# Kernel tuning notes

Measured on AMD Instinct MI355X. Metric: run time of the kernel, lower is better.

The kernel has to match this reference:

```python
import jax, jax.numpy as jnp
import numpy as np
import math

BLUR_RADIUS = 2.0


def _disk_kernel(radius):
    r = int(math.ceil(radius))
    ys, xs = np.mgrid[-r:r + 1, -r:r + 1]
    d = np.sqrt(xs * xs + ys * ys)
    w = np.clip(radius + 0.5 - d, 0.0, 1.0)
    w = w / w.sum()
    return jnp.asarray(w[None, None], jnp.float32)  # [1,1,k,k]


def transform_points(h, p, eps=1e-8):
    # h: [B,3,3], p: [P,2] -> [B,P,2]
    ph = jnp.concatenate([p, jnp.ones_like(p[:, :1])], axis=-1)
    pt = jnp.einsum('pj,bij->bpi', ph, h)
    z = pt[..., 2:]
    scale = jnp.where(jnp.abs(z) > eps, 1.0 / (z + eps), jnp.ones_like(z))
    return scale * pt[..., :2]


def grid_sample(img, grid):
    # img [C,Hi,Wi], grid [H,W,2] normalized, bilinear, zeros padding, align_corners=False
    C, Hi, Wi = img.shape
    gx = (grid[..., 0] + 1.0) * (Wi * 0.5) - 0.5
    gy = (grid[..., 1] + 1.0) * (Hi * 0.5) - 0.5
    x0 = jnp.floor(gx)
    y0 = jnp.floor(gy)
    wx = gx - x0
    wy = gy - y0

    def tap(xf, yf):
        ok = ((xf >= 0) & (xf < Wi) & (yf >= 0) & (yf < Hi)).astype(img.dtype)
        xi = jnp.clip(xf.astype(jnp.int32), 0, Wi - 1)
        yi = jnp.clip(yf.astype(jnp.int32), 0, Hi - 1)
        return img[:, yi, xi] * ok

    return (tap(x0, y0) * (1 - wx) * (1 - wy) + tap(x0 + 1, y0) * wx * (1 - wy)
            + tap(x0, y0 + 1) * (1 - wx) * wy + tap(x0 + 1, y0 + 1) * wx * wy)


def draw_patches(patches, homos, scale, kernel, H, W):
    n, c = patches.shape[:2]
    k = kernel.shape[-1]
    margin = k // 2
    corners = jnp.array([[-1., -1.], [1., -1.], [1., 1.], [-1., 1.]], jnp.float32)
    tpts = transform_points(homos, corners)  # [n,4,2]
    img_max = jnp.array([W, H], jnp.float32)
    lo = jnp.clip(jnp.min(tpts, axis=1) - margin, 0.0, img_max)  # [n,2] (x,y)
    hi = jnp.clip(jnp.max(tpts, axis=1) + margin, 0.0, img_max)
    # nearest upsample by static integer scale
    up = jnp.repeat(jnp.repeat(patches, scale, axis=2), scale, axis=3)
    alpha = jnp.ones_like(up)
    p = 2 * margin
    dw = jnp.broadcast_to(kernel, (c, 1, k, k))
    conv = lambda x: jax.lax.conv_general_dilated(x, dw, (1, 1), 'VALID', feature_group_count=c)
    fp = conv(jnp.pad(up, ((0, 0), (0, 0), (p, p), (p, p)), mode='edge'))
    fa = conv(jnp.pad(alpha, ((0, 0), (0, 0), (p, p), (p, p))))
    Hf, Wf = fp.shape[-2], fp.shape[-1]
    smtx = jnp.diag(jnp.array([(Wf - 2 * margin) / Wf, (Hf - 2 * margin) / Hf, 1.0], jnp.float32))
    hinv_s = jnp.einsum('ij,njk->nik', smtx, jnp.linalg.inv(homos))
    ys, xs = jnp.meshgrid(jnp.arange(H, dtype=jnp.float32), jnp.arange(W, dtype=jnp.float32), indexing='ij')
    coord = jnp.stack([xs + 0.5, ys + 0.5], axis=-1)  # [H,W,2]
    grid = transform_points(hinv_s, coord.reshape(-1, 2)).reshape(n, H, W, 2)
    ix0 = jnp.floor(lo).astype(jnp.int32)
    ix1 = jnp.floor(hi).astype(jnp.int32)
    xi = jnp.arange(W)
    yi = jnp.arange(H)
    inb = ((xi[None, None, :] >= ix0[:, None, None, 0]) & (xi[None, None, :] < ix1[:, None, None, 0])
           & (yi[None, :, None] >= ix0[:, None, None, 1]) & (yi[None, :, None] < ix1[:, None, None, 1]))
    grid = jnp.where(inb[..., None], grid, -2.0)  # -2 -> out of range -> zeros
    placed = jax.vmap(grid_sample)(fp, grid)
    palpha = jax.vmap(grid_sample)(fa, grid)
    return placed, palpha


def tdot(a, b):
    return jnp.sum(a * b, axis=1, keepdims=True)


def tnorm(m, eps=1e-8):
    l = jnp.maximum(jnp.sqrt(jnp.sum(m * m, axis=1, keepdims=True)), eps)
    return m / l


def render_specular(light_dir, view_dir, normals, roughness, fresnel=0.1, eps=1e-8):
    hv = tnorm((light_dir + view_dir) * 0.5, eps)
    NoH = jax.nn.relu(tdot(normals, hv))
    NoV = jax.nn.relu(tdot(normals, view_dir))
    NoL = jax.nn.relu(tdot(normals, light_dir))
    VoH = jax.nn.relu(tdot(view_dir, hv))
    alpha = roughness * roughness
    tmp = alpha / jnp.maximum(NoH * NoH * (alpha * alpha - 1.0) + 1.0, eps)
    D = tmp * tmp * (1.0 / np.pi)
    kk = alpha * 0.5
    G = NoL * NoV / jnp.maximum((NoL * (1.0 - kk) + kk) * (NoV * (1.0 - kk) + kk), eps)
    coeff = VoH * (-5.55473 * VoH - 6.98316)
    F_term = fresnel + (1.0 - fresnel) * jnp.exp2(coeff)
    f_s = D * G * F_term / jnp.maximum(4.0 * NoL * NoV, eps)
    return f_s * NoL * np.pi


def _unit(k, shape):
    v = jax.random.normal(k, shape, jnp.float32)
    return v / jnp.maximum(jnp.linalg.norm(v, axis=-1, keepdims=True), 1e-8)


def setup_inputs() -> dict:
    H, W, N, NB = 736, 1280, 8, 4
    key = jax.random.key(0)
    ks = jax.random.split(key, 12)
    rng = np.random.default_rng(0)

    def homos(n, lo, hi):
        hs = []
        for _ in range(n):
            s = rng.uniform(lo, hi)
            cx = rng.uniform(s + 10, W - s - 10)
            cy = rng.uniform(s + 10, H - s - 10)
            h = np.array([[s, rng.uniform(-0.05, 0.05) * s, cx],
                          [rng.uniform(-0.05, 0.05) * s, s, cy],
                          [rng.uniform(-3e-4, 3e-4), rng.uniform(-3e-4, 3e-4), 1.0]], np.float32)
            hs.append(h)
        return jnp.asarray(np.stack(hs))

    return {
        'image': jax.random.uniform(ks[0], (3, H, W), jnp.float32),
        'view_dirs': _unit(ks[1], (H, W, 3)),
        'markers': jax.random.uniform(ks[2], (N, 3, 64, 64), jnp.float32),
        'marker_h': homos(N, 50.0, 100.0),
        'board_h': homos(NB, 120.0, 220.0),
        'refl_dir': _unit(ks[3], (NB, 3)),
        'board_view_dir': _unit(ks[4], (NB, 3)),
        'board_normal': _unit(ks[5], (NB, 3)),
        'avg_color': jax.random.uniform(ks[6], (NB, 3), jnp.float32),
        'brightness_max': jax.random.uniform(ks[7], (NB, 1), jnp.float32),
        'roughness': 0.1 + 0.5 * jax.random.uniform(ks[8], (NB,), jnp.float32),
        'diffuse': jax.random.uniform(ks[9], (NB, 3), jnp.float32),
        'spec_scale': jax.random.uniform(ks[10], (NB,), jnp.float32),
        'normal_noise': 0.02 * jax.random.normal(ks[11], (3, H, W), jnp.float32),
        'marker_scale': 4,
        'board_scale': 128,
    }


def reference(image, view_dirs, markers, marker_h, board_h, refl_dir, board_view_dir,
              board_normal, avg_color, brightness_max, roughness, diffuse, spec_scale,
              normal_noise, marker_scale, board_scale):
    kernel = _disk_kernel(BLUR_RADIUS)
    H, W = image.shape[-2], image.shape[-1]
    nb = diffuse.shape[0]
    # specular normalization per board instance
    spec_max = render_specular(refl_dir, board_view_dir, board_normal,
                               jnp.broadcast_to(roughness[:, None], refl_dir.shape))  # [Nb,3]
    spec_power = avg_color / (jnp.max(spec_max, axis=1, keepdims=True) + 1e-8) * (1.1 - brightness_max)
    spec_power = spec_power * spec_scale[:, None]
    # warp markers and boards onto the image plane
    pm, pma = draw_patches(markers, marker_h, int(marker_scale), kernel, H, W)
    boards = jnp.broadcast_to(diffuse[:, :, None, None], (nb, 3, 4, 4))
    pb, pba = draw_patches(boards, board_h, int(board_scale), kernel, H, W)
    # per-pixel shading attribute maps
    hard = (pba != 0).astype(image.dtype)  # [Nb,3,H,W]
    sdirs = jnp.einsum('nchw,nc->chw', hard, refl_dir)
    snorm = jnp.einsum('nchw,nc->chw', hard, board_normal) + normal_noise
    rough_map = jnp.einsum('nchw,n->chw', hard, roughness)
    spow = jnp.einsum('nchw,nc->chw', pba, spec_power)
    snorm = tnorm(snorm[None])  # [1,3,H,W]
    pm_s, pma_s = pm.sum(0), pma.sum(0)
    pb_s, pba_s = pb.sum(0), pba.sum(0)
    stacked = pb_s * (1.0 - pma_s) + pb_s * pm_s * pma_s
    final = image * (1.0 - pba_s) + image * pba_s * stacked
    spec = render_specular(sdirs[None], jnp.transpose(view_dirs, (2, 0, 1))[None], snorm, rough_map[None])[0]
    return final + spec * spow
```

## Files before the change

### kernel.cpp

```cpp
#include <hip/hip_runtime.h>
#include <math.h>

#define HH 736
#define WW 1280
#define NPIX (HH*WW)
#define NM 8
#define NBRD 4
#define MS 260
#define BS 516

#define OFF_MINV 0
#define OFF_BBOX 108
#define OFF_SPOW 156
#define OFF_FAM  168
#define OFF_FAB  (OFF_FAM + MS*MS)
#define OFF_FP   (OFF_FAB + BS*BS)

struct K25 { float v[25]; };

__global__ void setup_kernel(const float* __restrict__ marker_h,
                             const float* __restrict__ board_h,
                             const float* __restrict__ refl,
                             const float* __restrict__ bview,
                             const float* __restrict__ bnorm,
                             const float* __restrict__ avg_color,
                             const float* __restrict__ bmax,
                             const float* __restrict__ rough,
                             const float* __restrict__ sscale,
                             float* __restrict__ minv_out,
                             int* __restrict__ bbox_out,
                             float* __restrict__ spow_out) {
  int t = threadIdx.x;
  if (t < 12) {
    const float* h = (t < NM) ? (marker_h + t*9) : (board_h + (t-NM)*9);
    double a=h[0],b=h[1],c=h[2],d=h[3],e=h[4],f=h[5],g=h[6],p=h[7],q=h[8];
    double A =  (e*q - f*p);
    double B = -(d*q - f*g);
    double C =  (d*p - e*g);
    double det = a*A + b*B + c*C;
    double id = 1.0/det;
    double inv[9];
    inv[0]= A*id;            inv[1]=-(b*q - c*p)*id;  inv[2]= (b*f - c*e)*id;
    inv[3]= B*id;            inv[4]= (a*q - c*g)*id;  inv[5]=-(a*f - c*d)*id;
    inv[6]= C*id;            inv[7]=-(a*p - b*g)*id;  inv[8]= (a*e - b*d)*id;
    float s0 = (t < NM) ? (float)(256.0/260.0) : (float)(512.0/516.0);
    minv_out[t*9+0]=(float)inv[0]*s0; minv_out[t*9+1]=(float)inv[1]*s0; minv_out[t*9+2]=(float)inv[2]*s0;
    minv_out[t*9+3]=(float)inv[3]*s0; minv_out[t*9+4]=(float)inv[4]*s0; minv_out[t*9+5]=(float)inv[5]*s0;
    minv_out[t*9+6]=(float)inv[6];    minv_out[t*9+7]=(float)inv[7];    minv_out[t*9+8]=(float)inv[8];
    const float cxs[4] = {-1.f, 1.f, 1.f, -1.f};
    const float cys[4] = {-1.f, -1.f, 1.f, 1.f};
    float mnx=1e30f, mny=1e30f, mxx=-1e30f, mxy=-1e30f;
    for (int k = 0; k < 4; ++k) {
      float X = h[0]*cxs[k] + h[1]*cys[k] + h[2];
      float Y = h[3]*cxs[k] + h[4]*cys[k] + h[5];
      float Z = h[6]*cxs[k] + h[7]*cys[k] + h[8];
      float sc = (fabsf(Z) > 1e-8f) ? 1.0f/(Z + 1e-8f) : 1.0f;
      float tx = X*sc, ty = Y*sc;
      mnx = fminf(mnx, tx); mny = fminf(mny, ty);
      mxx = fmaxf(mxx, tx); mxy = fmaxf(mxy, ty);
    }
    float lox = fminf(fmaxf(mnx - 2.0f, 0.f), (float)WW);
    float loy = fminf(fmaxf(mny - 2.0f, 0.f), (float)HH);
    float hix = fminf(fmaxf(mxx + 2.0f, 0.f), (float)WW);
    float hiy = fminf(fmaxf(mxy + 2.0f, 0.f), (float)HH);
    bbox_out[t*4+0] = (int)floorf(lox);
    bbox_out[t*4+1] = (int)floorf(loy);
    bbox_out[t*4+2] = (int)floorf(hix);
    bbox_out[t*4+3] = (int)floorf(hiy);
  }
  if (t >= 16 && t < 16 + NBRD) {
    int bidx = t - 16;
    float lx=refl[bidx*3+0], ly=refl[bidx*3+1], lz=refl[bidx*3+2];
    float vx=bview[bidx*3+0], vy=bview[bidx*3+1], vz=bview[bidx*3+2];
    float nx=bnorm[bidx*3+0], ny=bnorm[bidx*3+1], nz=bnorm[bidx*3+2];
    float r  = rough[bidx];
    float hx=(lx+vx)*0.5f, hy=(ly+vy)*0.5f, hz=(lz+vz)*0.5f;
    float hl=fmaxf(sqrtf(hx*hx+hy*hy+hz*hz), 1e-8f);
    hx/=hl; hy/=hl; hz/=hl;
    float NoH=fmaxf(0.f, nx*hx+ny*hy+nz*hz);
    float NoV=fmaxf(0.f, nx*vx+ny*vy+nz*vz);
    float NoL=fmaxf(0.f, nx*lx+ny*ly+nz*lz);
    float VoH=fmaxf(0.f, vx*hx+vy*hy+vz*hz);
    float al = r*r;
    float tmp = al / fmaxf(NoH*NoH*(al*al-1.f)+1.f, 1e-8f);
    float D = tmp*tmp*(float)(1.0/M_PI);
    float kk = al*0.5f;
    float G = NoL*NoV / fmaxf((NoL*(1.f-kk)+kk)*(NoV*(1.f-kk)+kk), 1e-8f);
    float co = VoH*(-5.55473f*VoH - 6.98316f);
    float F = 0.1f + 0.9f*exp2f(co);
    float f_s = D*G*F / fmaxf(4.f*NoL*NoV, 1e-8f);
    float smax = f_s*NoL*(float)M_PI;
    float invs = 1.0f/(smax + 1e-8f);
    float fac = (1.1f - bmax[bidx]) * sscale[bidx];
    spow_out[bidx*3+0] = avg_color[bidx*3+0]*invs*fac;
    spow_out[bidx*3+1] = avg_color[bidx*3+1]*invs*fac;
    spow_out[bidx*3+2] = avg_color[bidx*3+2]*invs*fac;
  }
}

__global__ __launch_bounds__(256) void marker_blur_kernel(
    const float* __restrict__ markers, float* __restrict__ fp, K25 K) {
  int idx = blockIdx.x*256 + threadIdx.x;
  if (idx >= NM*MS*MS) return;
  int x = idx % MS; int t = idx / MS; int y = t % MS; int n = t / MS;
  const float* p = markers + n*3*4096;
  float a0=0.f, a1=0.f, a2=0.f;
  #pragma unroll
  for (int ky = 0; ky < 5; ++ky) {
    int iy = y + ky - 4; iy = min(max(iy, 0), 255);
    int py = iy >> 2;
    #pragma unroll
    for (int kx = 0; kx < 5; ++kx) {
      int ix = x + kx - 4; ix = min(max(ix, 0), 255);
      int px = ix >> 2;
      float w = K.v[ky*5+kx];
      int o = py*64 + px;
      a0 += w * p[o];
      a1 += w * p[4096 + o];
      a2 += w * p[8192 + o];
    }
  }
  int o = idx*3;
  fp[o+0]=a0; fp[o+1]=a1; fp[o+2]=a2;
}

__global__ __launch_bounds__(256) void fa_kernel(float* __restrict__ out, int S, K25 K) {
  int idx = blockIdx.x*256 + threadIdx.x;
  if (idx >= S*S) return;
  int x = idx % S, y = idx / S;
  float a = 0.f;
  #pragma unroll
  for (int ky = 0; ky < 5; ++ky) {
    int iy = y + ky;
    bool oy = (iy >= 4) && (iy < S);
    #pragma unroll
    for (int kx = 0; kx < 5; ++kx) {
      int ix = x + kx;
      bool ox = (ix >= 4) && (ix < S);
      if (oy && ox) a += K.v[ky*5+kx];
    }
  }
  out[idx] = a;
}

__global__ __launch_bounds__(256) void main_kernel(
    const float* __restrict__ image, const float* __restrict__ vd,
    const float* __restrict__ noise, const float* __restrict__ diffuse,
    const float* __restrict__ refl, const float* __restrict__ bn,
    const float* __restrict__ rough, const float* __restrict__ minv,
    const int* __restrict__ bbox, const float* __restrict__ spow,
    const float* __restrict__ fp, const float* __restrict__ faM,
    const float* __restrict__ faB, float* __restrict__ out) {
  __shared__ float s_minv[108];
  __shared__ int   s_bbox[48];
  __shared__ float s_spow[12], s_refl[12], s_bn[12], s_diff[12], s_rough[4];
  int tid = threadIdx.x;
  if (tid < 108) s_minv[tid] = minv[tid];
  if (tid < 48)  s_bbox[tid] = bbox[tid];
  if (tid < 12) {
    s_spow[tid] = spow[tid]; s_refl[tid] = refl[tid];
    s_bn[tid]   = bn[tid];   s_diff[tid] = diffuse[tid];
  }
  if (tid < 4) s_rough[tid] = rough[tid];
  __syncthreads();

  int idx = blockIdx.x*256 + tid;
  int x = idx % WW, y = idx / WW;
  float pxc = (float)x + 0.5f, pyc = (float)y + 0.5f;

  float pm0=0.f, pm1=0.f, pm2=0.f, pma=0.f;
  for (int n = 0; n < NM; ++n) {
    const int* bb = &s_bbox[n*4];
    if (x < bb[0] || x >= bb[2] || y < bb[1] || y >= bb[3]) continue;
    const float* m = &s_minv[n*9];
    float X = m[0]*pxc + m[1]*pyc + m[2];
    float Y = m[3]*pxc + m[4]*pyc + m[5];
    float Z = m[6]*pxc + m[7]*pyc + m[8];
    float sc = (fabsf(Z) > 1e-8f) ? 1.0f/(Z + 1e-8f) : 1.0f;
    float gx = (X*sc + 1.0f)*(0.5f*MS) - 0.5f;
    float gy = (Y*sc + 1.0f)*(0.5f*MS) - 0.5f;
    float x0f = floorf(gx), y0f = floorf(gy);
    float wx = gx - x0f, wy = gy - y0f;
    int x0 = (int)x0f, y0 = (int)y0f, x1 = x0+1, y1 = y0+1;
    bool okx0 = (x0 >= 0) & (x0 < MS), okx1 = (x1 >= 0) & (x1 < MS);
    bool oky0 = (y0 >= 0) & (y0 < MS), oky1 = (y1 >= 0) & (y1 < MS);
    int cx0 = min(max(x0,0),MS-1), cx1 = min(max(x1,0),MS-1);
    int cy0 = min(max(y0,0),MS-1), cy1 = min(max(y1,0),MS-1);
    float w00 = (okx0&&oky0) ? (1.f-wx)*(1.f-wy) : 0.f;
    float w10 = (okx1&&oky0) ? wx*(1.f-wy)       : 0.f;
    float w01 = (okx0&&oky1) ? (1.f-wx)*wy       : 0.f;
    float w11 = (okx1&&oky1) ? wx*wy             : 0.f;
    int i00 = cy0*MS+cx0, i10 = cy0*MS+cx1, i01 = cy1*MS+cx0, i11 = cy1*MS+cx1;
    const float* f0 = fp + (size_t)n*MS*MS*3;
    const float* t00 = f0 + i00*3; const float* t10 = f0 + i10*3;
    const float* t01 = f0 + i01*3; const float* t11 = f0 + i11*3;
    pm0 += t00[0]*w00 + t10[0]*w10 + t01[0]*w01 + t11[0]*w11;
    pm1 += t00[1]*w00 + t10[1]*w10 + t01[1]*w01 + t11[1]*w11;
    pm2 += t00[2]*w00 + t10[2]*w10 + t01[2]*w01 + t11[2]*w11;
    pma += faM[i00]*w00 + faM[i10]*w10 + faM[i01]*w01 + faM[i11]*w11;
  }

  float pb0=0.f, pb1=0.f, pb2=0.f, pba=0.f;
  float sd0=0.f, sd1=0.f, sd2=0.f;
  float sn0=0.f, sn1=0.f, sn2=0.f;
  float rg=0.f, sp0=0.f, sp1=0.f, sp2=0.f;
  for (int n = 0; n < NBRD; ++n) {
    int b = NM + n;
    const int* bb = &s_bbox[b*4];
    if (x < bb[0] || x >= bb[2] || y < bb[1] || y >= bb[3]) continue;
    const float* m = &s_minv[b*9];
    float X = m[0]*pxc + m[1]*pyc + m[2];
    float Y = m[3]*pxc + m[4]*pyc + m[5];
    float Z = m[6]*pxc + m[7]*pyc + m[8];
    float sc = (fabsf(Z) > 1e-8f) ? 1.0f/(Z + 1e-8f) : 1.0f;
    float gx = (X*sc + 1.0f)*(0.5f*BS) - 0.5f;
    float gy = (Y*sc + 1.0f)*(0.5f*BS) - 0.5f;
    float x0f = floorf(gx), y0f = floorf(gy);
    float wx = gx - x0f, wy = gy - y0f;
    int x0 = (int)x0f, y0 = (int)y0f, x1 = x0+1, y1 = y0+1;
    bool okx0 = (x0 >= 0) & (x0 < BS), okx1 = (x1 >= 0) & (x1 < BS);
    bool oky0 = (y0 >= 0) & (y0 < BS), oky1 = (y1 >= 0) & (y1 < BS);
    int cx0 = min(max(x0,0),BS-1), cx1 = min(max(x1,0),BS-1);
    int cy0 = min(max(y0,0),BS-1), cy1 = min(max(y1,0),BS-1);
    float w00 = (okx0&&oky0) ? (1.f-wx)*(1.f-wy) : 0.f;
    float w10 = (okx1&&oky0) ? wx*(1.f-wy)       : 0.f;
    float w01 = (okx0&&oky1) ? (1.f-wx)*wy       : 0.f;
    float w11 = (okx1&&oky1) ? wx*wy             : 0.f;
    int i00 = cy0*BS+cx0, i10 = cy0*BS+cx1, i01 = cy1*BS+cx0, i11 = cy1*BS+cx1;
    float cov = w00 + w10 + w01 + w11;
    float pa  = faB[i00]*w00 + faB[i10]*w10 + faB[i01]*w01 + faB[i11]*w11;
    pb0 += s_diff[n*3+0]*cov;
    pb1 += s_diff[n*3+1]*cov;
    pb2 += s_diff[n*3+2]*cov;
    pba += pa;
    float hd = (pa != 0.f) ? 1.f : 0.f;
    sd0 += hd*s_refl[n*3+0]; sd1 += hd*s_refl[n*3+1]; sd2 += hd*s_refl[n*3+2];
    sn0 += hd*s_bn[n*3+0];   sn1 += hd*s_bn[n*3+1];   sn2 += hd*s_bn[n*3+2];
    rg  += hd*s_rough[n];
    sp0 += pa*s_spow[n*3+0]; sp1 += pa*s_spow[n*3+1]; sp2 += pa*s_spow[n*3+2];
  }

  float i0 = image[idx], i1 = image[NPIX+idx], i2 = image[2*NPIX+idx];
  float st0 = pb0*(1.f-pma) + pb0*pm0*pma;
  float st1 = pb1*(1.f-pma) + pb1*pm1*pma;
  float st2 = pb2*(1.f-pma) + pb2*pm2*pma;
  float fin0 = i0*(1.f-pba) + i0*pba*st0;
  float fin1 = i1*(1.f-pba) + i1*pba*st1;
  float fin2 = i2*(1.f-pba) + i2*pba*st2;

  float nx = sn0 + noise[idx];
  float ny = sn1 + noise[NPIX+idx];
  float nz = sn2 + noise[2*NPIX+idx];
  float nl = fmaxf(sqrtf(nx*nx+ny*ny+nz*nz), 1e-8f);
  nx /= nl; ny /= nl; nz /= nl;
  float vx = vd[idx*3+0], vy = vd[idx*3+1], vz = vd[idx*3+2];
  float hx = (sd0+vx)*0.5f, hy = (sd1+vy)*0.5f, hz = (sd2+vz)*0.5f;
  float hl = fmaxf(sqrtf(hx*hx+hy*hy+hz*hz), 1e-8f);
  hx /= hl; hy /= hl; hz /= hl;
  float NoH = fmaxf(0.f, nx*hx+ny*hy+nz*hz);
  float NoV = fmaxf(0.f, nx*vx+ny*vy+nz*vz);
  float NoL = fmaxf(0.f, nx*sd0+ny*sd1+nz*sd2);
  float VoH = fmaxf(0.f, vx*hx+vy*hy+vz*hz);
  float al = rg*rg;
  float tmp = al / fmaxf(NoH*NoH*(al*al-1.f)+1.f, 1e-8f);
  float D = tmp*tmp*(float)(1.0/M_PI);
  float kk = al*0.5f;
  float G = NoL*NoV / fmaxf((NoL*(1.f-kk)+kk)*(NoV*(1.f-kk)+kk), 1e-8f);
  float co = VoH*(-5.55473f*VoH - 6.98316f);
  float F = 0.1f + 0.9f*exp2f(co);
  float f_s = D*G*F / fmaxf(4.f*NoL*NoV, 1e-8f);
  float spec = f_s*NoL*(float)M_PI;

  out[idx]        = fin0 + spec*sp0;
  out[NPIX+idx]   = fin1 + spec*sp1;
  out[2*NPIX+idx] = fin2 + spec*sp2;
}

extern "C" void kernel_launch(void* const* d_in, const int* in_sizes, int n_in,
                              void* d_out, int out_size, void* d_ws, size_t ws_size,
                              hipStream_t stream) {
  const float* image    = (const float*)d_in[0];
  const float* vdirs    = (const float*)d_in[1];
  const float* markers  = (const float*)d_in[2];
  const float* marker_h = (const float*)d_in[3];
  const float* board_h  = (const float*)d_in[4];
  const float* refl     = (const float*)d_in[5];
  const float* bview    = (const float*)d_in[6];
  const float* bnorm    = (const float*)d_in[7];
  const float* avg_col  = (const float*)d_in[8];
  const float* bmax     = (const float*)d_in[9];
  const float* rough    = (const float*)d_in[10];
  const float* diffuse  = (const float*)d_in[11];
  const float* sscale   = (const float*)d_in[12];
  const float* noise    = (const float*)d_in[13];

  float* ws   = (float*)d_ws;
  float* minv = ws + OFF_MINV;
  int*   bbox = (int*)(ws + OFF_BBOX);
  float* spow = ws + OFF_SPOW;
  float* faM  = ws + OFF_FAM;
  float* faB  = ws + OFF_FAB;
  float* fp   = ws + OFF_FP;
  float* outp = (float*)d_out;

  K25 K;
  {
    double w[25]; double s = 0.0;
    for (int dy = -2; dy <= 2; ++dy)
      for (int dx = -2; dx <= 2; ++dx) {
        double d = sqrt((double)(dx*dx + dy*dy));
        double v = 2.5 - d;
        v = v < 0.0 ? 0.0 : (v > 1.0 ? 1.0 : v);
        w[(dy+2)*5 + (dx+2)] = v; s += v;
      }
    for (int i = 0; i < 25; ++i) K.v[i] = (float)(w[i]/s);
  }

  hipLaunchKernelGGL(setup_kernel, dim3(1), dim3(64), 0, stream,
                     marker_h, board_h, refl, bview, bnorm, avg_col, bmax,
                     rough, sscale, minv, bbox, spow);
  hipLaunchKernelGGL(marker_blur_kernel, dim3((NM*MS*MS + 255)/256), dim3(256), 0, stream,
                     markers, fp, K);
  hipLaunchKernelGGL(fa_kernel, dim3((MS*MS + 255)/256), dim3(256), 0, stream, faM, MS, K);
  hipLaunchKernelGGL(fa_kernel, dim3((BS*BS + 255)/256), dim3(256), 0, stream, faB, BS, K);
  hipLaunchKernelGGL(main_kernel, dim3(NPIX/256), dim3(256), 0, stream,
                     image, vdirs, noise, diffuse, refl, bnorm, rough,
                     minv, bbox, spow, fp, faM, faB, outp);
}
```

Baseline: 131.3 us.

## Merge precompute kernels into one launch and process four pixels per thread

The setup, marker blur and two alpha-coverage kernels are folded into a single precompute kernel that dispatches work by block index, cutting the launch count from five to two. The main kernel now handles four horizontally adjacent pixels per thread. It uses float4 loads for the image, noise and view directions and float4 stores for the output, and the bounding-box test is shared across the group. The aim is to reduce launch overhead and memory transaction count, at the cost of more registers per thread and fewer blocks in the main grid.

New measurement: 127.4 us. 1.03x faster.

```diff
diff --git a/kernel.cpp b/kernel.cpp
--- a/kernel.cpp
+++ b/kernel.cpp
@@ -16,131 +16,164 @@
 #define OFF_FAB  (OFF_FAM + MS*MS)
 #define OFF_FP   (OFF_FAB + BS*BS)
 
+#define BLUR_N (NM*MS*MS)
+#define BLUR_B ((BLUR_N + 255)/256)
+#define FAM_N  (MS*MS)
+#define FAM_B  ((FAM_N + 255)/256)
+#define FAB_N  (BS*BS)
+#define FAB_B  ((FAB_N + 255)/256)
+#define PRE_B  (1 + BLUR_B + FAM_B + FAB_B)
+
 struct K25 { float v[25]; };
 
-__global__ void setup_kernel(const float* __restrict__ marker_h,
-                             const float* __restrict__ board_h,
-                             const float* __restrict__ refl,
-                             const float* __restrict__ bview,
-                             const float* __restrict__ bnorm,
-                             const float* __restrict__ avg_color,
-                             const float* __restrict__ bmax,
-                             const float* __restrict__ rough,
-                             const float* __restrict__ sscale,
-                             float* __restrict__ minv_out,
-                             int* __restrict__ bbox_out,
-                             float* __restrict__ spow_out) {
-  int t = threadIdx.x;
-  if (t < 12) {
-    const float* h = (t < NM) ? (marker_h + t*9) : (board_h + (t-NM)*9);
-    double a=h[0],b=h[1],c=h[2],d=h[3],e=h[4],f=h[5],g=h[6],p=h[7],q=h[8];
-    double A =  (e*q - f*p);
-    double B = -(d*q - f*g);
-    double C =  (d*p - e*g);
-    double det = a*A + b*B + c*C;
-    double id = 1.0/det;
-    double inv[9];
-    inv[0]= A*id;            inv[1]=-(b*q - c*p)*id;  inv[2]= (b*f - c*e)*id;
-    inv[3]= B*id;            inv[4]= (a*q - c*g)*id;  inv[5]=-(a*f - c*d)*id;
-    inv[6]= C*id;            inv[7]=-(a*p - b*g)*id;  inv[8]= (a*e - b*d)*id;
-    float s0 = (t < NM) ? (float)(256.0/260.0) : (float)(512.0/516.0);
-    minv_out[t*9+0]=(float)inv[0]*s0; minv_out[t*9+1]=(float)inv[1]*s0; minv_out[t*9+2]=(float)inv[2]*s0;
-    minv_out[t*9+3]=(float)inv[3]*s0; minv_out[t*9+4]=(float)inv[4]*s0; minv_out[t*9+5]=(float)inv[5]*s0;
-    minv_out[t*9+6]=(float)inv[6];    minv_out[t*9+7]=(float)inv[7];    minv_out[t*9+8]=(float)inv[8];
-    const float cxs[4] = {-1.f, 1.f, 1.f, -1.f};
-    const float cys[4] = {-1.f, -1.f, 1.f, 1.f};
-    float mnx=1e30f, mny=1e30f, mxx=-1e30f, mxy=-1e30f;
-    for (int k = 0; k < 4; ++k) {
-      float X = h[0]*cxs[k] + h[1]*cys[k] + h[2];
-      float Y = h[3]*cxs[k] + h[4]*cys[k] + h[5];
-      float Z = h[6]*cxs[k] + h[7]*cys[k] + h[8];
-      float sc = (fabsf(Z) > 1e-8f) ? 1.0f/(Z + 1e-8f) : 1.0f;
-      float tx = X*sc, ty = Y*sc;
-      mnx = fminf(mnx, tx); mny = fminf(mny, ty);
-      mxx = fmaxf(mxx, tx); mxy = fmaxf(mxy, ty);
-    }
-    float lox = fminf(fmaxf(mnx - 2.0f, 0.f), (float)WW);
-    float loy = fminf(fmaxf(mny - 2.0f, 0.f), (float)HH);
-    float hix = fminf(fmaxf(mxx + 2.0f, 0.f), (float)WW);
-    float hiy = fminf(fmaxf(mxy + 2.0f, 0.f), (float)HH);
-    bbox_out[t*4+0] = (int)floorf(lox);
-    bbox_out[t*4+1] = (int)floorf(loy);
-    bbox_out[t*4+2] = (int)floorf(hix);
-    bbox_out[t*4+3] = (int)floorf(hiy);
-  }
-  if (t >= 16 && t < 16 + NBRD) {
-    int bidx = t - 16;
-    float lx=refl[bidx*3+0], ly=refl[bidx*3+1], lz=refl[bidx*3+2];
-    float vx=bview[bidx*3+0], vy=bview[bidx*3+1], vz=bview[bidx*3+2];
-    float nx=bnorm[bidx*3+0], ny=bnorm[bidx*3+1], nz=bnorm[bidx*3+2];
-    float r  = rough[bidx];
-    float hx=(lx+vx)*0.5f, hy=(ly+vy)*0.5f, hz=(lz+vz)*0.5f;
-    float hl=fmaxf(sqrtf(hx*hx+hy*hy+hz*hz), 1e-8f);
-    hx/=hl; hy/=hl; hz/=hl;
-    float NoH=fmaxf(0.f, nx*hx+ny*hy+nz*hz);
-    float NoV=fmaxf(0.f, nx*vx+ny*vy+nz*vz);
-    float NoL=fmaxf(0.f, nx*lx+ny*ly+nz*lz);
-    float VoH=fmaxf(0.f, vx*hx+vy*hy+vz*hz);
-    float al = r*r;
-    float tmp = al / fmaxf(NoH*NoH*(al*al-1.f)+1.f, 1e-8f);
-    float D = tmp*tmp*(float)(1.0/M_PI);
-    float kk = al*0.5f;
-    float G = NoL*NoV / fmaxf((NoL*(1.f-kk)+kk)*(NoV*(1.f-kk)+kk), 1e-8f);
-    float co = VoH*(-5.55473f*VoH - 6.98316f);
-    float F = 0.1f + 0.9f*exp2f(co);
-    float f_s = D*G*F / fmaxf(4.f*NoL*NoV, 1e-8f);
-    float smax = f_s*NoL*(float)M_PI;
-    float invs = 1.0f/(smax + 1e-8f);
-    float fac = (1.1f - bmax[bidx]) * sscale[bidx];
-    spow_out[bidx*3+0] = avg_color[bidx*3+0]*invs*fac;
-    spow_out[bidx*3+1] = avg_color[bidx*3+1]*invs*fac;
-    spow_out[bidx*3+2] = avg_color[bidx*3+2]*invs*fac;
-  }
-}
-
-__global__ __launch_bounds__(256) void marker_blur_kernel(
-    const float* __restrict__ markers, float* __restrict__ fp, K25 K) {
-  int idx = blockIdx.x*256 + threadIdx.x;
-  if (idx >= NM*MS*MS) return;
-  int x = idx % MS; int t = idx / MS; int y = t % MS; int n = t / MS;
-  const float* p = markers + n*3*4096;
-  float a0=0.f, a1=0.f, a2=0.f;
-  #pragma unroll
-  for (int ky = 0; ky < 5; ++ky) {
-    int iy = y + ky - 4; iy = min(max(iy, 0), 255);
-    int py = iy >> 2;
-    #pragma unroll
-    for (int kx = 0; kx < 5; ++kx) {
-      int ix = x + kx - 4; ix = min(max(ix, 0), 255);
-      int px = ix >> 2;
-      float w = K.v[ky*5+kx];
-      int o = py*64 + px;
-      a0 += w * p[o];
-      a1 += w * p[4096 + o];
-      a2 += w * p[8192 + o];
-    }
-  }
-  int o = idx*3;
-  fp[o+0]=a0; fp[o+1]=a1; fp[o+2]=a2;
-}
-
-__global__ __launch_bounds__(256) void fa_kernel(float* __restrict__ out, int S, K25 K) {
-  int idx = blockIdx.x*256 + threadIdx.x;
-  if (idx >= S*S) return;
-  int x = idx % S, y = idx / S;
-  float a = 0.f;
-  #pragma unroll
-  for (int ky = 0; ky < 5; ++ky) {
-    int iy = y + ky;
-    bool oy = (iy >= 4) && (iy < S);
-    #pragma unroll
-    for (int kx = 0; kx < 5; ++kx) {
-      int ix = x + kx;
-      bool ox = (ix >= 4) && (ix < S);
-      if (oy && ox) a += K.v[ky*5+kx];
-    }
-  }
-  out[idx] = a;
+__global__ __launch_bounds__(256) void precompute_kernel(
+    const float* __restrict__ markers,
+    const float* __restrict__ marker_h, const float* __restrict__ board_h,
+    const float* __restrict__ refl, const float* __restrict__ bview,
+    const float* __restrict__ bnorm, const float* __restrict__ avg_color,
+    const float* __restrict__ bmax, const float* __restrict__ rough,
+    const float* __restrict__ sscale,
+    float* __restrict__ minv_out, int* __restrict__ bbox_out,
+    float* __restrict__ spow_out, float* __restrict__ fp,
+    float* __restrict__ faM, float* __restrict__ faB, K25 K) {
+  int b = blockIdx.x;
+  int tid = threadIdx.x;
+
+  if (b == 0) {
+    int t = tid;
+    if (t < 12) {
+      const float* h = (t < NM) ? (marker_h + t*9) : (board_h + (t-NM)*9);
+      double a=h[0],bb=h[1],c=h[2],d=h[3],e=h[4],f=h[5],g=h[6],p=h[7],q=h[8];
+      double A =  (e*q - f*p);
+      double B = -(d*q - f*g);
+      double C =  (d*p - e*g);
+      double det = a*A + bb*B + c*C;
+      double id = 1.0/det;
+      double inv[9];
+      inv[0]= A*id;             inv[1]=-(bb*q - c*p)*id;  inv[2]= (bb*f - c*e)*id;
+      inv[3]= B*id;             inv[4]= (a*q - c*g)*id;   inv[5]=-(a*f - c*d)*id;
+      inv[6]= C*id;             inv[7]=-(a*p - bb*g)*id;  inv[8]= (a*e - bb*d)*id;
+      float s0 = (t < NM) ? (float)(256.0/260.0) : (float)(512.0/516.0);
+      minv_out[t*9+0]=(float)inv[0]*s0; minv_out[t*9+1]=(float)inv[1]*s0; minv_out[t*9+2]=(float)inv[2]*s0;
+      minv_out[t*9+3]=(float)inv[3]*s0; minv_out[t*9+4]=(float)inv[4]*s0; minv_out[t*9+5]=(float)inv[5]*s0;
+      minv_out[t*9+6]=(float)inv[6];    minv_out[t*9+7]=(float)inv[7];    minv_out[t*9+8]=(float)inv[8];
+      const float cxs[4] = {-1.f, 1.f, 1.f, -1.f};
+      const float cys[4] = {-1.f, -1.f, 1.f, 1.f};
+      float mnx=1e30f, mny=1e30f, mxx=-1e30f, mxy=-1e30f;
+      for (int k = 0; k < 4; ++k) {
+        float X = h[0]*cxs[k] + h[1]*cys[k] + h[2];
+        float Y = h[3]*cxs[k] + h[4]*cys[k] + h[5];
+        float Z = h[6]*cxs[k] + h[7]*cys[k] + h[8];
+        float sc = (fabsf(Z) > 1e-8f) ? 1.0f/(Z + 1e-8f) : 1.0f;
+        float tx = X*sc, ty = Y*sc;
+        mnx = fminf(mnx, tx); mny = fminf(mny, ty);
+        mxx = fmaxf(mxx, tx); mxy = fmaxf(mxy, ty);
+      }
+      float lox = fminf(fmaxf(mnx - 2.0f, 0.f), (float)WW);
+      float loy = fminf(fmaxf(mny - 2.0f, 0.f), (float)HH);
+      float hix = fminf(fmaxf(mxx + 2.0f, 0.f), (float)WW);
+      float hiy = fminf(fmaxf(mxy + 2.0f, 0.f), (float)HH);
+      bbox_out[t*4+0] = (int)floorf(lox);
+      bbox_out[t*4+1] = (int)floorf(loy);
+      bbox_out[t*4+2] = (int)floorf(hix);
+      bbox_out[t*4+3] = (int)floorf(hiy);
+    }
+    if (t >= 16 && t < 16 + NBRD) {
+      int bi = t - 16;
+      float lx=refl[bi*3+0], ly=refl[bi*3+1], lz=refl[bi*3+2];
+      float vx=bview[bi*3+0], vy=bview[bi*3+1], vz=bview[bi*3+2];
+      float nx=bnorm[bi*3+0], ny=bnorm[bi*3+1], nz=bnorm[bi*3+2];
+      float r  = rough[bi];
+      float hx=(lx+vx)*0.5f, hy=(ly+vy)*0.5f, hz=(lz+vz)*0.5f;
+      float hl=fmaxf(sqrtf(hx*hx+hy*hy+hz*hz), 1e-8f);
+      hx/=hl; hy/=hl; hz/=hl;
+      float NoH=fmaxf(0.f, nx*hx+ny*hy+nz*hz);
+      float NoV=fmaxf(0.f, nx*vx+ny*vy+nz*vz);
+      float NoL=fmaxf(0.f, nx*lx+ny*ly+nz*lz);
+      float VoH=fmaxf(0.f, vx*hx+vy*hy+vz*hz);
+      float al = r*r;
+      float tmp = al / fmaxf(NoH*NoH*(al*al-1.f)+1.f, 1e-8f);
+      float D = tmp*tmp*(float)(1.0/M_PI);
+      float kk = al*0.5f;
+      float G = NoL*NoV / fmaxf((NoL*(1.f-kk)+kk)*(NoV*(1.f-kk)+kk), 1e-8f);
+      float co = VoH*(-5.55473f*VoH - 6.98316f);
+      float F = 0.1f + 0.9f*exp2f(co);
+      float f_s = D*G*F / fmaxf(4.f*NoL*NoV, 1e-8f);
+      float smax = f_s*NoL*(float)M_PI;
+      float invs = 1.0f/(smax + 1e-8f);
+      float fac = (1.1f - bmax[bi]) * sscale[bi];
+      spow_out[bi*3+0] = avg_color[bi*3+0]*invs*fac;
+      spow_out[bi*3+1] = avg_color[bi*3+1]*invs*fac;
+      spow_out[bi*3+2] = avg_color[bi*3+2]*invs*fac;
+    }
+    return;
+  }
+
+  if (b < 1 + BLUR_B) {
+    int idx = (b-1)*256 + tid;
+    if (idx >= BLUR_N) return;
+    int x = idx % MS; int t = idx / MS; int y = t % MS; int n = t / MS;
+    const float* p = markers + n*3*4096;
+    float a0=0.f, a1=0.f, a2=0.f;
+    #pragma unroll
+    for (int ky = 0; ky < 5; ++ky) {
+      int iy = y + ky - 4; iy = min(max(iy, 0), 255);
+      int py = iy >> 2;
+      #pragma unroll
+      for (int kx = 0; kx < 5; ++kx) {
+        int ix = x + kx - 4; ix = min(max(ix, 0), 255);
+        int px = ix >> 2;
+        float w = K.v[ky*5+kx];
+        int o = py*64 + px;
+        a0 += w * p[o];
+        a1 += w * p[4096 + o];
+        a2 += w * p[8192 + o];
+      }
+    }
+    int o = idx*3;
+    fp[o+0]=a0; fp[o+1]=a1; fp[o+2]=a2;
+    return;
+  }
+
+  if (b < 1 + BLUR_B + FAM_B) {
+    int idx = (b-1-BLUR_B)*256 + tid;
+    if (idx >= FAM_N) return;
+    int x = idx % MS, y = idx / MS;
+    float a = 0.f;
+    #pragma unroll
+    for (int ky = 0; ky < 5; ++ky) {
+      int iy = y + ky;
+      bool oy = (iy >= 4) && (iy < MS);
+      #pragma unroll
+      for (int kx = 0; kx < 5; ++kx) {
+        int ix = x + kx;
+        bool ox = (ix >= 4) && (ix < MS);
+        if (oy && ox) a += K.v[ky*5+kx];
+      }
+    }
+    faM[idx] = a;
+    return;
+  }
+
+  {
+    int idx = (b-1-BLUR_B-FAM_B)*256 + tid;
+    if (idx >= FAB_N) return;
+    int x = idx % BS, y = idx / BS;
+    float a = 0.f;
+    #pragma unroll
+    for (int ky = 0; ky < 5; ++ky) {
+      int iy = y + ky;
+      bool oy = (iy >= 4) && (iy < BS);
+      #pragma unroll
+      for (int kx = 0; kx < 5; ++kx) {
+        int ix = x + kx;
+        bool ox = (ix >= 4) && (ix < BS);
+        if (oy && ox) a += K.v[ky*5+kx];
+      }
+    }
+    faB[idx] = a;
+    return;
+  }
 }
 
 __global__ __launch_bounds__(256) void main_kernel(
@@ -164,116 +197,146 @@
   if (tid < 4) s_rough[tid] = rough[tid];
   __syncthreads();
 
-  int idx = blockIdx.x*256 + tid;
-  int x = idx % WW, y = idx / WW;
-  float pxc = (float)x + 0.5f, pyc = (float)y + 0.5f;
-
-  float pm0=0.f, pm1=0.f, pm2=0.f, pma=0.f;
+  int base = (blockIdx.x*256 + tid)*4;
+  int x0i = base % WW;
+  int y   = base / WW;
+  float pyc = (float)y + 0.5f;
+
+  float pm0[4]={0,0,0,0}, pm1[4]={0,0,0,0}, pm2[4]={0,0,0,0}, pma[4]={0,0,0,0};
   for (int n = 0; n < NM; ++n) {
     const int* bb = &s_bbox[n*4];
-    if (x < bb[0] || x >= bb[2] || y < bb[1] || y >= bb[3]) continue;
+    if (y < bb[1] || y >= bb[3] || x0i+3 < bb[0] || x0i >= bb[2]) continue;
     const float* m = &s_minv[n*9];
-    float X = m[0]*pxc + m[1]*pyc + m[2];
-    float Y = m[3]*pxc + m[4]*pyc + m[5];
-    float Z = m[6]*pxc + m[7]*pyc + m[8];
-    float sc = (fabsf(Z) > 1e-8f) ? 1.0f/(Z + 1e-8f) : 1.0f;
-    float gx = (X*sc + 1.0f)*(0.5f*MS) - 0.5f;
-    float gy = (Y*sc + 1.0f)*(0.5f*MS) - 0.5f;
-    float x0f = floorf(gx), y0f = floorf(gy);
-    float wx = gx - x0f, wy = gy - y0f;
-    int x0 = (int)x0f, y0 = (int)y0f, x1 = x0+1, y1 = y0+1;
-    bool okx0 = (x0 >= 0) & (x0 < MS), okx1 = (x1 >= 0) & (x1 < MS);
-    bool oky0 = (y0 >= 0) & (y0 < MS), oky1 = (y1 >= 0) & (y1 < MS);
-    int cx0 = min(max(x0,0),MS-1), cx1 = min(max(x1,0),MS-1);
-    int cy0 = min(max(y0,0),MS-1), cy1 = min(max(y1,0),MS-1);
-    float w00 = (okx0&&oky0) ? (1.f-wx)*(1.f-wy) : 0.f;
-    float w10 = (okx1&&oky0) ? wx*(1.f-wy)       : 0.f;
-    float w01 = (okx0&&oky1) ? (1.f-wx)*wy       : 0.f;
-    float w11 = (okx1&&oky1) ? wx*wy             : 0.f;
-    int i00 = cy0*MS+cx0, i10 = cy0*MS+cx1, i01 = cy1*MS+cx0, i11 = cy1*MS+cx1;
-    const float* f0 = fp + (size_t)n*MS*MS*3;
-    const float* t00 = f0 + i00*3; const float* t10 = f0 + i10*3;
-    const float* t01 = f0 + i01*3; const float* t11 = f0 + i11*3;
-    pm0 += t00[0]*w00 + t10[0]*w10 + t01[0]*w01 + t11[0]*w11;
-    pm1 += t00[1]*w00 + t10[1]*w10 + t01[1]*w01 + t11[1]*w11;
-    pm2 += t00[2]*w00 + t10[2]*w10 + t01[2]*w01 + t11[2]*w11;
-    pma += faM[i00]*w00 + faM[i10]*w10 + faM[i01]*w01 + faM[i11]*w11;
-  }
-
-  float pb0=0.f, pb1=0.f, pb2=0.f, pba=0.f;
-  float sd0=0.f, sd1=0.f, sd2=0.f;
-  float sn0=0.f, sn1=0.f, sn2=0.f;
-  float rg=0.f, sp0=0.f, sp1=0.f, sp2=0.f;
+    #pragma unroll
+    for (int k = 0; k < 4; ++k) {
+      int x = x0i + k;
+      if (x < bb[0] || x >= bb[2]) continue;
+      float pxc = (float)x + 0.5f;
+      float X = m[0]*pxc + m[1]*pyc + m[2];
+      float Y = m[3]*pxc + m[4]*pyc + m[5];
+      float Z = m[6]*pxc + m[7]*pyc + m[8];
+      float sc = (fabsf(Z) > 1e-8f) ? 1.0f/(Z + 1e-8f) : 1.0f;
+      float gx = (X*sc + 1.0f)*(0.5f*MS) - 0.5f;
+      float gy = (Y*sc + 1.0f)*(0.5f*MS) - 0.5f;
+      float x0f = floorf(gx), y0f = floorf(gy);
+      float wx = gx - x0f, wy = gy - y0f;
+      int ix0 = (int)x0f, iy0 = (int)y0f, ix1 = ix0+1, iy1 = iy0+1;
+      bool okx0 = (ix0 >= 0) & (ix0 < MS), okx1 = (ix1 >= 0) & (ix1 < MS);
+      bool oky0 = (iy0 >= 0) & (iy0 < MS), oky1 = (iy1 >= 0) & (iy1 < MS);
+      int cx0 = min(max(ix0,0),MS-1), cx1 = min(max(ix1,0),MS-1);
+      int cy0 = min(max(iy0,0),MS-1), cy1 = min(max(iy1,0),MS-1);
+      float w00 = (okx0&&oky0) ? (1.f-wx)*(1.f-wy) : 0.f;
+      float w10 = (okx1&&oky0) ? wx*(1.f-wy)       : 0.f;
+      float w01 = (okx0&&oky1) ? (1.f-wx)*wy       : 0.f;
+      float w11 = (okx1&&oky1) ? wx*wy             : 0.f;
+      int i00 = cy0*MS+cx0, i10 = cy0*MS+cx1, i01 = cy1*MS+cx0, i11 = cy1*MS+cx1;
+      const float* f0 = fp + (size_t)n*MS*MS*3;
+      const float* t00 = f0 + i00*3; const float* t10 = f0 + i10*3;
+      const float* t01 = f0 + i01*3; const float* t11 = f0 + i11*3;
+      pm0[k] += t00[0]*w00 + t10[0]*w10 + t01[0]*w01 + t11[0]*w11;
+      pm1[k] += t00[1]*w00 + t10[1]*w10 + t01[1]*w01 + t11[1]*w11;
+      pm2[k] += t00[2]*w00 + t10[2]*w10 + t01[2]*w01 + t11[2]*w11;
+      pma[k] += faM[i00]*w00 + faM[i10]*w10 + faM[i01]*w01 + faM[i11]*w11;
+    }
+  }
+
+  float pb0[4]={0,0,0,0}, pb1[4]={0,0,0,0}, pb2[4]={0,0,0,0}, pba[4]={0,0,0,0};
+  float sd0[4]={0,0,0,0}, sd1[4]={0,0,0,0}, sd2[4]={0,0,0,0};
+  float sn0[4]={0,0,0,0}, sn1[4]={0,0,0,0}, sn2[4]={0,0,0,0};
+  float rg[4]={0,0,0,0},  sp0[4]={0,0,0,0}, sp1[4]={0,0,0,0}, sp2[4]={0,0,0,0};
   for (int n = 0; n < NBRD; ++n) {
-    int b = NM + n;
-    const int* bb = &s_bbox[b*4];
-    if (x < bb[0] || x >= bb[2] || y < bb[1] || y >= bb[3]) continue;
-    const float* m = &s_minv[b*9];
-    float X = m[0]*pxc + m[1]*pyc + m[2];
-    float Y = m[3]*pxc + m[4]*pyc + m[5];
-    float Z = m[6]*pxc + m[7]*pyc + m[8];
-    float sc = (fabsf(Z) > 1e-8f) ? 1.0f/(Z + 1e-8f) : 1.0f;
-    float gx = (X*sc + 1.0f)*(0.5f*BS) - 0.5f;
-    float gy = (Y*sc + 1.0f)*(0.5f*BS) - 0.5f;
-    float x0f = floorf(gx), y0f = floorf(gy);
-    float wx = gx - x0f, wy = gy - y0f;
-    int x0 = (int)x0f, y0 = (int)y0f, x1 = x0+1, y1 = y0+1;
-    bool okx0 = (x0 >= 0) & (x0 < BS), okx1 = (x1 >= 0) & (x1 < BS);
-    bool oky0 = (y0 >= 0) & (y0 < BS), oky1 = (y1 >= 0) & (y1 < BS);
-    int cx0 = min(max(x0,0),BS-1), cx1 = min(max(x1,0),BS-1);
-    int cy0 = min(max(y0,0),BS-1), cy1 = min(max(y1,0),BS-1);
-    float w00 = (okx0&&oky0) ? (1.f-wx)*(1.f-wy) : 0.f;
-    float w10 = (okx1&&oky0) ? wx*(1.f-wy)       : 0.f;
-    float w01 = (okx0&&oky1) ? (1.f-wx)*wy       : 0.f;
-    float w11 = (okx1&&oky1) ? wx*wy             : 0.f;
-    int i00 = cy0*BS+cx0, i10 = cy0*BS+cx1, i01 = cy1*BS+cx0, i11 = cy1*BS+cx1;
-    float cov = w00 + w10 + w01 + w11;
-    float pa  = faB[i00]*w00 + faB[i10]*w10 + faB[i01]*w01 + faB[i11]*w11;
-    pb0 += s_diff[n*3+0]*cov;
-    pb1 += s_diff[n*3+1]*cov;
-    pb2 += s_diff[n*3+2]*cov;
-    pba += pa;
-    float hd = (pa != 0.f) ? 1.f : 0.f;
-    sd0 += hd*s_refl[n*3+0]; sd1 += hd*s_refl[n*3+1]; sd2 += hd*s_refl[n*3+2];
-    sn0 += hd*s_bn[n*3+0];   sn1 += hd*s_bn[n*3+1];   sn2 += hd*s_bn[n*3+2];
-    rg  += hd*s_rough[n];
-    sp0 += pa*s_spow[n*3+0]; sp1 += pa*s_spow[n*3+1]; sp2 += pa*s_spow[n*3+2];
-  }
-
-  float i0 = image[idx], i1 = image[NPIX+idx], i2 = image[2*NPIX+idx];
-  float st0 = pb0*(1.f-pma) + pb0*pm0*pma;
-  float st1 = pb1*(1.f-pma) + pb1*pm1*pma;
-  float st2 = pb2*(1.f-pma) + pb2*pm2*pma;
-  float fin0 = i0*(1.f-pba) + i0*pba*st0;
-  float fin1 = i1*(1.f-pba) + i1*pba*st1;
-  float fin2 = i2*(1.f-pba) + i2*pba*st2;
-
-  float nx = sn0 + noise[idx];
-  float ny = sn1 + noise[NPIX+idx];
-  float nz = sn2 + noise[2*NPIX+idx];
-  float nl = fmaxf(sqrtf(nx*nx+ny*ny+nz*nz), 1e-8f);
-  nx /= nl; ny /= nl; nz /= nl;
-  float vx = vd[idx*3+0], vy = vd[idx*3+1], vz = vd[idx*3+2];
-  float hx = (sd0+vx)*0.5f, hy = (sd1+vy)*0.5f, hz = (sd2+vz)*0.5f;
-  float hl = fmaxf(sqrtf(hx*hx+hy*hy+hz*hz), 1e-8f);
-  hx /= hl; hy /= hl; hz /= hl;
-  float NoH = fmaxf(0.f, nx*hx+ny*hy+nz*hz);
-  float NoV = fmaxf(0.f, nx*vx+ny*vy+nz*vz);
-  float NoL = fmaxf(0.f, nx*sd0+ny*sd1+nz*sd2);
-  float VoH = fmaxf(0.f, vx*hx+vy*hy+vz*hz);
-  float al = rg*rg;
-  float tmp = al / fmaxf(NoH*NoH*(al*al-1.f)+1.f, 1e-8f);
-  float D = tmp*tmp*(float)(1.0/M_PI);
-  float kk = al*0.5f;
-  float G = NoL*NoV / fmaxf((NoL*(1.f-kk)+kk)*(NoV*(1.f-kk)+kk), 1e-8f);
-  float co = VoH*(-5.55473f*VoH - 6.98316f);
-  float F = 0.1f + 0.9f*exp2f(co);
-  float f_s = D*G*F / fmaxf(4.f*NoL*NoV, 1e-8f);
-  float spec = f_s*NoL*(float)M_PI;
-
-  out[idx]        = fin0 + spec*sp0;
-  out[NPIX+idx]   = fin1 + spec*sp1;
-  out[2*NPIX+idx] = fin2 + spec*sp2;
+    int bix = NM + n;
+    const int* bb = &s_bbox[bix*4];
+    if (y < bb[1] || y >= bb[3] || x0i+3 < bb[0] || x0i >= bb[2]) continue;
+    const float* m = &s_minv[bix*9];
+    #pragma unroll
+    for (int k = 0; k < 4; ++k) {
+      int x = x0i + k;
+      if (x < bb[0] || x >= bb[2]) continue;
+      float pxc = (float)x + 0.5f;
+      float X = m[0]*pxc + m[1]*pyc + m[2];
+      float Y = m[3]*pxc + m[4]*pyc + m[5];
+      float Z = m[6]*pxc + m[7]*pyc + m[8];
+      float sc = (fabsf(Z) > 1e-8f) ? 1.0f/(Z + 1e-8f) : 1.0f;
+      float gx = (X*sc + 1.0f)*(0.5f*BS) - 0.5f;
+      float gy = (Y*sc + 1.0f)*(0.5f*BS) - 0.5f;
+      float x0f = floorf(gx), y0f = floorf(gy);
+      float wx = gx - x0f, wy = gy - y0f;
+      int ix0 = (int)x0f, iy0 = (int)y0f, ix1 = ix0+1, iy1 = iy0+1;
+      bool okx0 = (ix0 >= 0) & (ix0 < BS), okx1 = (ix1 >= 0) & (ix1 < BS);
+      bool oky0 = (iy0 >= 0) & (iy0 < BS), oky1 = (iy1 >= 0) & (iy1 < BS);
+      int cx0 = min(max(ix0,0),BS-1), cx1 = min(max(ix1,0),BS-1);
+      int cy0 = min(max(iy0,0),BS-1), cy1 = min(max(iy1,0),BS-1);
+      float w00 = (okx0&&oky0) ? (1.f-wx)*(1.f-wy) : 0.f;
+      float w10 = (okx1&&oky0) ? wx*(1.f-wy)       : 0.f;
+      float w01 = (okx0&&oky1) ? (1.f-wx)*wy       : 0.f;
+      float w11 = (okx1&&oky1) ? wx*wy             : 0.f;
+      int i00 = cy0*BS+cx0, i10 = cy0*BS+cx1, i01 = cy1*BS+cx0, i11 = cy1*BS+cx1;
+      float cov = w00 + w10 + w01 + w11;
+      float pa  = faB[i00]*w00 + faB[i10]*w10 + faB[i01]*w01 + faB[i11]*w11;
+      pb0[k] += s_diff[n*3+0]*cov;
+      pb1[k] += s_diff[n*3+1]*cov;
+      pb2[k] += s_diff[n*3+2]*cov;
+      pba[k] += pa;
+      float hd = (pa != 0.f) ? 1.f : 0.f;
+      sd0[k] += hd*s_refl[n*3+0]; sd1[k] += hd*s_refl[n*3+1]; sd2[k] += hd*s_refl[n*3+2];
+      sn0[k] += hd*s_bn[n*3+0];   sn1[k] += hd*s_bn[n*3+1];   sn2[k] += hd*s_bn[n*3+2];
+      rg[k]  += hd*s_rough[n];
+      sp0[k] += pa*s_spow[n*3+0]; sp1[k] += pa*s_spow[n*3+1]; sp2[k] += pa*s_spow[n*3+2];
+    }
+  }
+
+  float i0a[4], i1a[4], i2a[4], n0a[4], n1a[4], n2a[4], vdl[12];
+  *(float4*)i0a = *(const float4*)(image + base);
+  *(float4*)i1a = *(const float4*)(image + NPIX + base);
+  *(float4*)i2a = *(const float4*)(image + 2*NPIX + base);
+  *(float4*)n0a = *(const float4*)(noise + base);
+  *(float4*)n1a = *(const float4*)(noise + NPIX + base);
+  *(float4*)n2a = *(const float4*)(noise + 2*NPIX + base);
+  *(float4*)&vdl[0] = *(const float4*)(vd + (size_t)base*3);
+  *(float4*)&vdl[4] = *(const float4*)(vd + (size_t)base*3 + 4);
+  *(float4*)&vdl[8] = *(const float4*)(vd + (size_t)base*3 + 8);
+
+  float o0a[4], o1a[4], o2a[4];
+  #pragma unroll
+  for (int k = 0; k < 4; ++k) {
+    float st0 = pb0[k]*(1.f-pma[k]) + pb0[k]*pm0[k]*pma[k];
+    float st1 = pb1[k]*(1.f-pma[k]) + pb1[k]*pm1[k]*pma[k];
+    float st2 = pb2[k]*(1.f-pma[k]) + pb2[k]*pm2[k]*pma[k];
+    float fin0 = i0a[k]*(1.f-pba[k]) + i0a[k]*pba[k]*st0;
+    float fin1 = i1a[k]*(1.f-pba[k]) + i1a[k]*pba[k]*st1;
+    float fin2 = i2a[k]*(1.f-pba[k]) + i2a[k]*pba[k]*st2;
+
+    float nx = sn0[k] + n0a[k];
+    float ny = sn1[k] + n1a[k];
+    float nz = sn2[k] + n2a[k];
+    float nl = fmaxf(sqrtf(nx*nx+ny*ny+nz*nz), 1e-8f);
+    nx /= nl; ny /= nl; nz /= nl;
+    float vx = vdl[3*k+0], vy = vdl[3*k+1], vz = vdl[3*k+2];
+    float hx = (sd0[k]+vx)*0.5f, hy = (sd1[k]+vy)*0.5f, hz = (sd2[k]+vz)*0.5f;
+    float hl = fmaxf(sqrtf(hx*hx+hy*hy+hz*hz), 1e-8f);
+    hx /= hl; hy /= hl; hz /= hl;
+    float NoH = fmaxf(0.f, nx*hx+ny*hy+nz*hz);
+    float NoV = fmaxf(0.f, nx*vx+ny*vy+nz*vz);
+    float NoL = fmaxf(0.f, nx*sd0[k]+ny*sd1[k]+nz*sd2[k]);
+    float VoH = fmaxf(0.f, vx*hx+vy*hy+vz*hz);
+    float al = rg[k]*rg[k];
+    float tmp = al / fmaxf(NoH*NoH*(al*al-1.f)+1.f, 1e-8f);
+    float D = tmp*tmp*(float)(1.0/M_PI);
+    float kk = al*0.5f;
+    float G = NoL*NoV / fmaxf((NoL*(1.f-kk)+kk)*(NoV*(1.f-kk)+kk), 1e-8f);
+    float co = VoH*(-5.55473f*VoH - 6.98316f);
+    float F = 0.1f + 0.9f*exp2f(co);
+    float f_s = D*G*F / fmaxf(4.f*NoL*NoV, 1e-8f);
+    float spec = f_s*NoL*(float)M_PI;
+
+    o0a[k] = fin0 + spec*sp0[k];
+    o1a[k] = fin1 + spec*sp1[k];
+    o2a[k] = fin2 + spec*sp2[k];
+  }
+  *(float4*)(out + base)          = *(float4*)o0a;
+  *(float4*)(out + NPIX + base)   = *(float4*)o1a;
+  *(float4*)(out + 2*NPIX + base) = *(float4*)o2a;
 }
 
 extern "C" void kernel_launch(void* const* d_in, const int* in_sizes, int n_in,
@@ -316,14 +379,10 @@
     for (int i = 0; i < 25; ++i) K.v[i] = (float)(w[i]/s);
   }
 
-  hipLaunchKernelGGL(setup_kernel, dim3(1), dim3(64), 0, stream,
-                     marker_h, board_h, refl, bview, bnorm, avg_col, bmax,
-                     rough, sscale, minv, bbox, spow);
-  hipLaunchKernelGGL(marker_blur_kernel, dim3((NM*MS*MS + 255)/256), dim3(256), 0, stream,
-                     markers, fp, K);
-  hipLaunchKernelGGL(fa_kernel, dim3((MS*MS + 255)/256), dim3(256), 0, stream, faM, MS, K);
-  hipLaunchKernelGGL(fa_kernel, dim3((BS*BS + 255)/256), dim3(256), 0, stream, faB, BS, K);
-  hipLaunchKernelGGL(main_kernel, dim3(NPIX/256), dim3(256), 0, stream,
+  hipLaunchKernelGGL(precompute_kernel, dim3(PRE_B), dim3(256), 0, stream,
+                     markers, marker_h, board_h, refl, bview, bnorm, avg_col,
+                     bmax, rough, sscale, minv, bbox, spow, fp, faM, faB, K);
+  hipLaunchKernelGGL(main_kernel, dim3(NPIX/1024), dim3(256), 0, stream,
                      image, vdirs, noise, diffuse, refl, bnorm, rough,
                      minv, bbox, spow, fp, faM, faB, outp);
 }
```
